# Kernel tuning notes

Hardware: AMD Instinct MI355X
Metric: run time of the kernel (lower is better)

Reference implementation:

```python
import jax, jax.numpy as jnp
import numpy as np
import math

EMBED = 512
KDIM = 512
VDIM = 512
H = 8
HD = EMBED // H
N = 2048
L = 2048
B = 4


def setup_inputs() -> dict:
    key = jax.random.key(0)
    ks = jax.random.split(key, 14)
    s = 1.0 / math.sqrt(EMBED)
    return {
        "q": jax.random.normal(ks[0], (N, B, EMBED), jnp.float32),
        "k": jax.random.normal(ks[1], (L, B, KDIM), jnp.float32),
        "v": jax.random.normal(ks[2], (L, B, VDIM), jnp.float32),
        "pe1": jax.random.normal(ks[3], (B, N, 3), jnp.float32),
        "pe2": jax.random.normal(ks[4], (L, 3), jnp.float32),
        "Wq": jax.random.normal(ks[5], (EMBED, EMBED), jnp.float32) * s,
        "bq": jnp.zeros((EMBED,), jnp.float32),
        "Wk": jax.random.normal(ks[6], (EMBED, KDIM), jnp.float32) * s,
        "bk": jnp.zeros((EMBED,), jnp.float32),
        "Wv": jax.random.normal(ks[7], (EMBED, VDIM), jnp.float32) * s,
        "bv": jnp.zeros((EMBED,), jnp.float32),
        "Wo": jax.random.normal(ks[8], (EMBED, EMBED), jnp.float32) * s,
        "bo": jnp.zeros((EMBED,), jnp.float32),
    }


def reference(q, k, v, pe1, pe2, Wq, bq, Wk, bk, Wv, bv, Wo, bo):
    n, b, _ = q.shape
    l = k.shape[0]
    # projections (nn.Linear: x @ W.T + b)
    qp = q @ Wq.T + bq  # (n, b, E)
    kp = k @ Wk.T + bk  # (l, b, E)
    vp = v @ Wv.T + bv  # (l, b, E)
    # split heads -> (b, H, n, hd)
    qh = qp.reshape(n, b, H, HD).transpose(1, 2, 0, 3)
    kh = kp.reshape(l, b, H, HD).transpose(1, 2, 0, 3)
    vh = vp.reshape(l, b, H, HD).transpose(1, 2, 0, 3)
    # relative PE bias: (b, n, l), broadcast over heads
    pe_scores = jnp.einsum('bnc,lc->bnl', pe1, pe2)[:, None, :, :]
    scores = (jnp.einsum('bhnd,bhld->bhnl', qh, kh) + pe_scores) / math.sqrt(HD)
    attn = jax.nn.softmax(scores, axis=-1)
    out = jnp.einsum('bhnl,bhld->bhnd', attn, vh)  # (b, H, n, hd)
    out = out.transpose(2, 0, 1, 3).reshape(n, b, EMBED)
    return out @ Wo.T + bo
```

## Files before the change

kernel.cpp:

```cpp
#include <hip/hip_runtime.h>
#include <math.h>

#define EMBED 512
#define HDIM 64
#define NHEADS 8
#define SEQ_N 2048
#define SEQ_L 2048
#define BATCH 4
#define MROWS (SEQ_N*BATCH)
#define BE (BATCH*EMBED)

#define QSCALE 0.18033688f

typedef _Float16 f16;
typedef _Float16 half8 __attribute__((ext_vector_type(8)));
typedef _Float16 half4 __attribute__((ext_vector_type(4)));
typedef _Float16 half2v __attribute__((ext_vector_type(2)));
typedef float floatx4 __attribute__((ext_vector_type(4)));
typedef float floatx16 __attribute__((ext_vector_type(16)));

static __device__ inline float fast_exp2(float x) {
#if __has_builtin(__builtin_amdgcn_exp2f)
  return __builtin_amdgcn_exp2f(x);
#else
  return __expf(x * 0.69314718056f);
#endif
}

static __device__ inline half2v pk2(float a, float b) {
#if __has_builtin(__builtin_amdgcn_cvt_pkrtz)
  return __builtin_bit_cast(half2v, __builtin_amdgcn_cvt_pkrtz(a, b));
#else
  half2v o; o[0] = (f16)a; o[1] = (f16)b; return o;
#endif
}

static __device__ inline void gload16(const void* g, void* l) {
  __builtin_amdgcn_global_load_lds(
      (__attribute__((address_space(1))) void*)(g),
      (__attribute__((address_space(3))) void*)(l), 16, 0, 0);
}

__global__ __launch_bounds__(256) void cvt_all(const float* __restrict__ q,
                                               const float* __restrict__ k,
                                               const float* __restrict__ v,
                                               const float* __restrict__ Wq,
                                               const float* __restrict__ Wk,
                                               const float* __restrict__ Wv,
                                               const float* __restrict__ Wo,
                                               f16* __restrict__ qb, f16* __restrict__ kb,
                                               f16* __restrict__ vb, f16* __restrict__ Wb) {
  const long TOK = (long)MROWS * EMBED;
  const long WSZ = (long)EMBED * EMBED;
  int y = blockIdx.y;
  long i = ((long)blockIdx.x * 256 + threadIdx.x) * 4;
  if (y < 3) {
    if (i < TOK) {
      const float* s = y == 0 ? q : y == 1 ? k : v;
      f16* d = y == 0 ? qb : y == 1 ? kb : vb;
      float4 f = *reinterpret_cast<const float4*>(s + i);
      half4 o; o[0] = (f16)f.x; o[1] = (f16)f.y; o[2] = (f16)f.z; o[3] = (f16)f.w;
      *reinterpret_cast<half4*>(d + i) = o;
    }
  } else {
    if (i < 4 * WSZ) {
      int sel = (int)(i >> 18);
      long off = i & (WSZ - 1);
      const float* s = sel == 0 ? Wq : sel == 1 ? Wk : sel == 2 ? Wv : Wo;
      float4 f = *reinterpret_cast<const float4*>(s + off);
      half4 o; o[0] = (f16)f.x; o[1] = (f16)f.y; o[2] = (f16)f.z; o[3] = (f16)f.w;
      *reinterpret_cast<half4*>(Wb + i) = o;
    }
  }
}

__global__ __launch_bounds__(256) void gemm_qkv(const f16* __restrict__ A0,
                                                const f16* __restrict__ A1,
                                                const f16* __restrict__ A2,
                                                const f16* __restrict__ W0,
                                                const f16* __restrict__ W1,
                                                const f16* __restrict__ W2,
                                                const float* __restrict__ b0,
                                                const float* __restrict__ b1,
                                                const float* __restrict__ b2,
                                                f16* __restrict__ C0, f16* __restrict__ C1,
                                                f16* __restrict__ C2t) {
  __shared__ alignas(16) unsigned char gsm[34816];
  f16* As = reinterpret_cast<f16*>(gsm);
  f16* Bs = reinterpret_cast<f16*>(gsm + 16384);
  f16* T  = reinterpret_cast<f16*>(gsm);
  const int sel = blockIdx.y >> 2;
  const f16* A = sel == 0 ? A0 : sel == 1 ? A1 : A2;
  const f16* Bt = sel == 0 ? W0 : sel == 1 ? W1 : W2;
  const float* bias = sel == 0 ? b0 : sel == 1 ? b1 : b2;
  const float scl = sel == 0 ? QSCALE : 1.0f;
  const int tid = threadIdx.x;
  const int wave = tid >> 6, lane = tid & 63, quad = lane >> 4, l16 = lane & 15;
  const int wm = wave & 1, wn = wave >> 1;
  const long m0 = (long)blockIdx.x * 128;
  const long n0 = (long)(blockIdx.y & 3) * 128;
  const int srow = lane >> 2;
  const int scol = (lane & 3) * 8;

  const f16* Ag0 = A + (m0 + wave * 32 + srow) * EMBED + scol;
  const f16* Ag1 = A + (m0 + wave * 32 + 16 + srow) * EMBED + scol;
  const f16* Bg0 = Bt + (n0 + wave * 32 + srow) * EMBED + scol;
  const f16* Bg1 = Bt + (n0 + wave * 32 + 16 + srow) * EMBED + scol;

  gload16(Ag0, &As[(wave * 32) * 32]);
  gload16(Ag1, &As[(wave * 32 + 16) * 32]);
  gload16(Bg0, &Bs[(wave * 32) * 32]);
  gload16(Bg1, &Bs[(wave * 32 + 16) * 32]);
  floatx4 acc[4][4] = {};
  asm volatile("s_waitcnt vmcnt(0)" ::: "memory");
  __builtin_amdgcn_s_barrier();

#pragma unroll
  for (int ks = 0; ks < 16; ++ks) {
    const int cur = ks & 1;
    if (ks + 1 < 16) {
      const int k1 = (ks + 1) * 32;
      gload16(Ag0 + k1, &As[(cur ^ 1) * 4096 + (wave * 32) * 32]);
      gload16(Ag1 + k1, &As[(cur ^ 1) * 4096 + (wave * 32 + 16) * 32]);
      gload16(Bg0 + k1, &Bs[(cur ^ 1) * 4096 + (wave * 32) * 32]);
      gload16(Bg1 + k1, &Bs[(cur ^ 1) * 4096 + (wave * 32 + 16) * 32]);
    }
    half8 af[4], bf[4];
#pragma unroll
    for (int i = 0; i < 4; ++i)
      af[i] = *reinterpret_cast<const half8*>(&As[cur * 4096 + (wm * 64 + i * 16 + l16) * 32 + quad * 8]);
#pragma unroll
    for (int j = 0; j < 4; ++j)
      bf[j] = *reinterpret_cast<const half8*>(&Bs[cur * 4096 + (wn * 64 + j * 16 + l16) * 32 + quad * 8]);
#pragma unroll
    for (int i = 0; i < 4; ++i)
#pragma unroll
      for (int j = 0; j < 4; ++j)
        acc[i][j] = __builtin_amdgcn_mfma_f32_16x16x32_f16(af[i], bf[j], acc[i][j], 0, 0, 0);
    if (ks + 1 < 16) {
      asm volatile("s_waitcnt vmcnt(0)" ::: "memory");
      __builtin_amdgcn_s_barrier();
    }
  }

  if (sel != 2) {
    f16* C = sel == 0 ? C0 : C1;
#pragma unroll
    for (int i = 0; i < 4; ++i)
#pragma unroll
      for (int r = 0; r < 4; ++r) {
        long row = m0 + wm * 64 + i * 16 + quad * 4 + r;
#pragma unroll
        for (int j = 0; j < 4; ++j) {
          long col = n0 + wn * 64 + j * 16 + l16;
          float val = (acc[i][j][r] + bias[col]) * scl;
          C[row * EMBED + col] = (f16)val;
        }
      }
  } else {
    __syncthreads();
#pragma unroll
    for (int i = 0; i < 4; ++i)
#pragma unroll
      for (int r = 0; r < 4; ++r) {
        int mrow = wm * 64 + i * 16 + quad * 4 + r;
        int bq = mrow & 3, lt = mrow >> 2;
#pragma unroll
        for (int j = 0; j < 4; ++j) {
          int col = wn * 64 + j * 16 + l16;
          float val = acc[i][j][r] + bias[n0 + col];
          T[col * 136 + bq * 32 + lt] = (f16)val;
        }
      }
    __syncthreads();
    const int h0 = (int)(n0 >> 6);
    const long lbase = m0 >> 2;
#pragma unroll
    for (int it = 0; it < 8; ++it) {
      int f = it * 256 + tid;
      int ls = f & 3, bq = (f >> 2) & 3, d6 = (f >> 4) & 63, hl = f >> 10;
      half8 o = *reinterpret_cast<const half8*>(&T[(hl * 64 + d6) * 136 + bq * 32 + ls * 8]);
      *reinterpret_cast<half8*>(C2t + (((long)bq * 8 + h0 + hl) * 64 + d6) * 2048 + lbase + ls * 8) = o;
    }
  }
}

__global__ __launch_bounds__(256) void gemm_out(const f16* __restrict__ A,
                                                const f16* __restrict__ Bt,
                                                const float* __restrict__ bias,
                                                float* __restrict__ C) {
  __shared__ alignas(16) f16 As[2][128 * 32];
  __shared__ alignas(16) f16 Bs[2][64 * 32];
  const int tid = threadIdx.x;
  const int wave = tid >> 6, lane = tid & 63, quad = lane >> 4, l16 = lane & 15;
  const long m0 = (long)blockIdx.x * 128;
  const long n0 = (long)blockIdx.y * 64;
  const int srow = lane >> 2;
  const int scol = (lane & 3) * 8;

  const f16* Ag0 = A + (m0 + wave * 32 + srow) * EMBED + scol;
  const f16* Ag1 = A + (m0 + wave * 32 + 16 + srow) * EMBED + scol;
  const f16* Bg0 = Bt + (n0 + wave * 16 + srow) * EMBED + scol;

  gload16(Ag0, &As[0][(wave * 32) * 32]);
  gload16(Ag1, &As[0][(wave * 32 + 16) * 32]);
  gload16(Bg0, &Bs[0][(wave * 16) * 32]);
  floatx4 acc[2][4] = {};
  asm volatile("s_waitcnt vmcnt(0)" ::: "memory");
  __builtin_amdgcn_s_barrier();

#pragma unroll
  for (int ks = 0; ks < 16; ++ks) {
    const int cur = ks & 1;
    if (ks + 1 < 16) {
      const int k1 = (ks + 1) * 32;
      gload16(Ag0 + k1, &As[cur ^ 1][(wave * 32) * 32]);
      gload16(Ag1 + k1, &As[cur ^ 1][(wave * 32 + 16) * 32]);
      gload16(Bg0 + k1, &Bs[cur ^ 1][(wave * 16) * 32]);
    }
    half8 af[2], bf[4];
#pragma unroll
    for (int i = 0; i < 2; ++i)
      af[i] = *reinterpret_cast<const half8*>(&As[cur][(wave * 32 + i * 16 + l16) * 32 + quad * 8]);
#pragma unroll
    for (int j = 0; j < 4; ++j)
      bf[j] = *reinterpret_cast<const half8*>(&Bs[cur][(j * 16 + l16) * 32 + quad * 8]);
#pragma unroll
    for (int i = 0; i < 2; ++i)
#pragma unroll
      for (int j = 0; j < 4; ++j)
        acc[i][j] = __builtin_amdgcn_mfma_f32_16x16x32_f16(af[i], bf[j], acc[i][j], 0, 0, 0);
    if (ks + 1 < 16) {
      asm volatile("s_waitcnt vmcnt(0)" ::: "memory");
      __builtin_amdgcn_s_barrier();
    }
  }
#pragma unroll
  for (int i = 0; i < 2; ++i)
#pragma unroll
    for (int r = 0; r < 4; ++r) {
      long row = m0 + wave * 32 + i * 16 + quad * 4 + r;
#pragma unroll
      for (int j = 0; j < 4; ++j) {
        long col = n0 + j * 16 + l16;
        C[row * EMBED + col] = acc[i][j][r] + bias[col];
      }
    }
}

#define KBUFB (128 * 64 * 2)
#define VBUFB (64 * 128 * 2)
#define PEBUFB (128 * 16 * 2)
#define LDSB (2 * KBUFB + 2 * VBUFB + 2 * PEBUFB)
#define NCHUNK (SEQ_L / 128)
__global__ __launch_bounds__(512, 4) void attn_flash(const f16* __restrict__ qp,
                                                     const f16* __restrict__ kp,
                                                     const f16* __restrict__ vt,
                                                     const float* __restrict__ pe1,
                                                     const float* __restrict__ pe2,
                                                     f16* __restrict__ ao) {
  __shared__ alignas(16) unsigned char smem[LDSB];
  f16* K0 = reinterpret_cast<f16*>(smem);
  f16* V0 = reinterpret_cast<f16*>(smem + 2 * KBUFB);
  f16* P0 = reinterpret_cast<f16*>(smem + 2 * KBUFB + 2 * VBUFB);
  float* comb = reinterpret_cast<float*>(smem);
  const int tid = threadIdx.x, wave = tid >> 6, lane = tid & 63;
  const int m = lane & 31, h = lane >> 5;
  const int strip = wave & 3, half = wave >> 2;
  const int W = blockIdx.y * 16 + blockIdx.x;
  const int bh = (W & 7) + ((W >> 7) << 3);
  const int n0 = ((W >> 3) & 15) * 128;
  const int b = bh >> 3, hd = bh & 7;
  const long headoff = (long)b * EMBED + hd * HDIM;
  const long vhead = (long)bh * 64 * 2048;

  const int krow0 = wave * 16 + (lane >> 3);
  const int kg = (lane & 7) ^ (lane >> 3);
  const f16* ksrc0 = kp + headoff + (long)krow0 * BE + kg * 8;
  const int vd0 = wave * 8 + (lane >> 4);
  const int vd1 = vd0 + 4;
  const int vg0 = (lane & 15) ^ (vd0 & 7);
  const int vg1 = (lane & 15) ^ (vd1 & 7);
  const f16* vsrc0 = vt + vhead + (long)vd0 * 2048 + vg0 * 8;
  const f16* vsrc1 = vt + vhead + (long)vd1 * 2048 + vg1 * 8;

  for (int c = tid; c < 1024; c += 512) {
    int r = c >> 3, col = (c & 7) * 8;
    *reinterpret_cast<uint4*>(&K0[r * 64 + col]) =
        *reinterpret_cast<const uint4*>(qp + (long)(n0 + r) * BE + headoff + col);
  }
  gload16(vsrc0, V0 + wave * 1024);
  gload16(vsrc1, V0 + wave * 1024 + 512);
  if (tid < 256) {
    const uint2 z2 = {0, 0};
    const uint4 z4 = {0, 0, 0, 0};
    *reinterpret_cast<uint2*>(reinterpret_cast<char*>(P0) + tid * 32 + 8) = z2;
    *reinterpret_cast<uint4*>(reinterpret_cast<char*>(P0) + tid * 32 + 16) = z4;
  }
  if (tid < 128) {
    long base = ((long)b * SEQ_N + n0 + tid) * 3;
    half4 v8;
    v8[0] = (f16)(pe1[base + 0] * QSCALE);
    v8[1] = (f16)(pe1[base + 1] * QSCALE);
    v8[2] = (f16)(pe1[base + 2] * QSCALE);
    v8[3] = (f16)0.f;
    *reinterpret_cast<half4*>(&P0[tid * 16]) = v8;
  }
  __syncthreads();

  half8 qf[5];
#pragma unroll
  for (int e = 0; e < 4; ++e)
    qf[e] = *reinterpret_cast<const half8*>(&K0[(strip * 32 + m) * 64 + e * 16 + h * 8]);
  qf[4] = *reinterpret_cast<const half8*>(&P0[(strip * 32 + m) * 16 + h * 8]);
  __syncthreads();

  gload16(ksrc0, K0 + wave * 1024);
  gload16(ksrc0 + 8 * BE, K0 + wave * 1024 + 512);
  {
    int pr = tid & 127;
    float a0 = pe2[(long)pr * 3 + 0];
    float a1 = pe2[(long)pr * 3 + 1];
    float a2 = pe2[(long)pr * 3 + 2];
    if (tid < 128) {
      half4 p2v; p2v[0] = (f16)a0; p2v[1] = (f16)a1; p2v[2] = (f16)a2; p2v[3] = (f16)0.f;
      *reinterpret_cast<half4*>(&P0[tid * 16]) = p2v;
    }
  }
  __syncthreads();

  floatx16 oacc[2] = {};
  float lpart = 0.f;

  auto compute_chunk = [&](int bsel) {
    const f16* Kb = K0 + bsel * 8192;
    const f16* Vb = V0 + bsel * 8192;
    const f16* Pb = P0 + bsel * 2048;
#pragma unroll
    for (int tt = 0; tt < 2; ++tt) {
      const int t = half * 2 + tt;
      const int row = t * 32 + m;
      const int r7 = m & 7;
      floatx16 st = {};
#pragma unroll
      for (int e = 0; e < 4; ++e) {
        half8 kf = *reinterpret_cast<const half8*>(&Kb[row * 64 + (((2 * e + h) ^ r7) * 8)]);
        st = __builtin_amdgcn_mfma_f32_32x32x16_f16(kf, qf[e], st, 0, 0, 0);
      }
      {
        half8 kf = *reinterpret_cast<const half8*>(&Pb[row * 16 + h * 8]);
        st = __builtin_amdgcn_mfma_f32_32x32x16_f16(kf, qf[4], st, 0, 0, 0);
      }
      float p[16];
#pragma unroll
      for (int r = 0; r < 16; ++r) {
        p[r] = fast_exp2(st[r]);
        lpart += p[r];
      }
#pragma unroll
      for (int s = 0; s < 4; ++s) {
        half2v u0 = pk2(p[4 * s + 0], p[4 * s + 1]);
        half2v u1 = pk2(p[4 * s + 2], p[4 * s + 3]);
        half4 bp;
        bp[0] = u0[0]; bp[1] = u0[1]; bp[2] = u1[0]; bp[3] = u1[1];
        const int sl = t * 4 + s;
#pragma unroll
        for (int dt = 0; dt < 2; ++dt) {
          const int d = dt * 32 + m;
          half4 vf = *reinterpret_cast<const half4*>(&Vb[d * 128 + ((sl ^ r7) * 8) + h * 4]);
          oacc[dt] = __builtin_amdgcn_mfma_f32_32x32x8f16(vf, bp, oacc[dt], 0, 0, 0);
        }
      }
    }
  };

  int buf = 0;
#pragma unroll 1
  for (int c = 0; c < NCHUNK - 1; ++c) {
    const int l0n = (c + 1) * 128;
    f16* Kn = K0 + (buf ^ 1) * 8192;
    f16* Vn = V0 + (buf ^ 1) * 8192;
    gload16(ksrc0 + (long)l0n * BE, Kn + wave * 1024);
    gload16(ksrc0 + (long)l0n * BE + 8 * BE, Kn + wave * 1024 + 512);
    gload16(vsrc0 + l0n, Vn + wave * 1024);
    gload16(vsrc1 + l0n, Vn + wave * 1024 + 512);
    int pr = tid & 127;
    float a0 = pe2[(long)(l0n + pr) * 3 + 0];
    float a1 = pe2[(long)(l0n + pr) * 3 + 1];
    float a2 = pe2[(long)(l0n + pr) * 3 + 2];

    __builtin_amdgcn_s_setprio(1);
    compute_chunk(buf);
    __builtin_amdgcn_s_setprio(0);

    if (tid < 128) {
      half4 p2v; p2v[0] = (f16)a0; p2v[1] = (f16)a1; p2v[2] = (f16)a2; p2v[3] = (f16)0.f;
      *reinterpret_cast<half4*>(&P0[(buf ^ 1) * 2048 + tid * 16]) = p2v;
    }
    __syncthreads();
    buf ^= 1;
  }
  __builtin_amdgcn_s_setprio(1);
  compute_chunk(buf);
  __builtin_amdgcn_s_setprio(0);
  __syncthreads();

  lpart += __shfl_xor(lpart, 32);

  if (half == 1) {
    float* dst = comb + (strip * 64 + lane) * 33;
#pragma unroll
    for (int dt = 0; dt < 2; ++dt)
#pragma unroll
      for (int x = 0; x < 16; ++x) dst[dt * 16 + x] = oacc[dt][x];
    dst[32] = lpart;
  }
  __syncthreads();
  if (half == 0) {
    const float* src = comb + (strip * 64 + lane) * 33;
#pragma unroll
    for (int dt = 0; dt < 2; ++dt)
#pragma unroll
      for (int x = 0; x < 16; ++x) oacc[dt][x] += src[dt * 16 + x];
    float inv = 1.f / (lpart + src[32]);
    long qrow = n0 + strip * 32 + m;
#pragma unroll
    for (int dt = 0; dt < 2; ++dt)
#pragma unroll
      for (int g = 0; g < 4; ++g) {
        half4 o4;
#pragma unroll
        for (int x = 0; x < 4; ++x) o4[x] = (f16)(oacc[dt][4 * g + x] * inv);
        int d = dt * 32 + 8 * g + 4 * h;
        *reinterpret_cast<half4*>(ao + qrow * BE + headoff + d) = o4;
      }
  }
}

extern "C" void kernel_launch(void* const* d_in, const int* in_sizes, int n_in,
                              void* d_out, int out_size, void* d_ws, size_t ws_size,
                              hipStream_t stream) {
  const float* q   = (const float*)d_in[0];
  const float* k   = (const float*)d_in[1];
  const float* v   = (const float*)d_in[2];
  const float* pe1 = (const float*)d_in[3];
  const float* pe2 = (const float*)d_in[4];
  const float* Wq  = (const float*)d_in[5];
  const float* bq  = (const float*)d_in[6];
  const float* Wk  = (const float*)d_in[7];
  const float* bk  = (const float*)d_in[8];
  const float* Wv  = (const float*)d_in[9];
  const float* bv  = (const float*)d_in[10];
  const float* Wo  = (const float*)d_in[11];
  const float* bo  = (const float*)d_in[12];
  float* out = (float*)d_out;

  f16* ws = (f16*)d_ws;
  const long TOK = (long)MROWS * EMBED;
  const long WSZ = (long)EMBED * EMBED;
  f16* qb  = ws;
  f16* kb  = qb + TOK;
  f16* vb  = kb + TOK;
  f16* Wqb = vb + TOK;
  f16* Wkb = Wqb + WSZ;
  f16* Wvb = Wkb + WSZ;
  f16* Wob = Wvb + WSZ;
  f16* qpb = Wob + WSZ;
  f16* kpb = qpb + TOK;
  f16* vtb = kpb + TOK;
  f16* aob = vtb + TOK;

  cvt_all<<<dim3(4096, 4), 256, 0, stream>>>(q, k, v, Wq, Wk, Wv, Wo, qb, kb, vb, Wqb);

  gemm_qkv<<<dim3(MROWS / 128, 12), 256, 0, stream>>>(qb, kb, vb, Wqb, Wkb, Wvb,
                                                      bq, bk, bv, qpb, kpb, vtb);

  attn_flash<<<dim3(SEQ_N / 128, BATCH * NHEADS), 512, 0, stream>>>(qpb, kpb, vtb, pe1, pe2, aob);

  gemm_out<<<dim3(MROWS / 128, EMBED / 64), 256, 0, stream>>>(aob, Wob, bo, out);
}
```

Baseline: 197.6 us.

## Fuse fp32-to-fp16 activation conversion into QKV GEMM loads

The QKV projection GEMM now reads the fp32 q/k/v activations directly into registers, converts them to fp16 and stores them into LDS. The separate conversion pass over the activations and its fp16 round trip through global memory are gone, leaving a small weight-only conversion kernel. Each GEMM block now re-reads fp32 A tiles, so with 4 column blocks per matrix that traffic repeats 4 times, and the A-tile pipeline moves from async global-to-LDS loads to register-staged stores. The s_setprio calls around the attention compute are also removed.

```diff
diff --git a/kernel.cpp b/kernel.cpp
--- a/kernel.cpp
+++ b/kernel.cpp
@@ -35,48 +35,39 @@
 #endif
 }
 
+static __device__ inline half8 cvt8(float4 u, float4 v) {
+  half2v p0 = pk2(u.x, u.y), p1 = pk2(u.z, u.w);
+  half2v p2 = pk2(v.x, v.y), p3 = pk2(v.z, v.w);
+  half8 o;
+  o[0] = p0[0]; o[1] = p0[1]; o[2] = p1[0]; o[3] = p1[1];
+  o[4] = p2[0]; o[5] = p2[1]; o[6] = p3[0]; o[7] = p3[1];
+  return o;
+}
+
 static __device__ inline void gload16(const void* g, void* l) {
   __builtin_amdgcn_global_load_lds(
       (__attribute__((address_space(1))) void*)(g),
       (__attribute__((address_space(3))) void*)(l), 16, 0, 0);
 }
 
-__global__ __launch_bounds__(256) void cvt_all(const float* __restrict__ q,
-                                               const float* __restrict__ k,
-                                               const float* __restrict__ v,
-                                               const float* __restrict__ Wq,
-                                               const float* __restrict__ Wk,
-                                               const float* __restrict__ Wv,
-                                               const float* __restrict__ Wo,
-                                               f16* __restrict__ qb, f16* __restrict__ kb,
-                                               f16* __restrict__ vb, f16* __restrict__ Wb) {
-  const long TOK = (long)MROWS * EMBED;
+__global__ __launch_bounds__(256) void cvt_w(const float* __restrict__ Wq,
+                                             const float* __restrict__ Wk,
+                                             const float* __restrict__ Wv,
+                                             const float* __restrict__ Wo,
+                                             f16* __restrict__ Wb) {
   const long WSZ = (long)EMBED * EMBED;
-  int y = blockIdx.y;
   long i = ((long)blockIdx.x * 256 + threadIdx.x) * 4;
-  if (y < 3) {
-    if (i < TOK) {
-      const float* s = y == 0 ? q : y == 1 ? k : v;
-      f16* d = y == 0 ? qb : y == 1 ? kb : vb;
-      float4 f = *reinterpret_cast<const float4*>(s + i);
-      half4 o; o[0] = (f16)f.x; o[1] = (f16)f.y; o[2] = (f16)f.z; o[3] = (f16)f.w;
-      *reinterpret_cast<half4*>(d + i) = o;
-    }
-  } else {
-    if (i < 4 * WSZ) {
-      int sel = (int)(i >> 18);
-      long off = i & (WSZ - 1);
-      const float* s = sel == 0 ? Wq : sel == 1 ? Wk : sel == 2 ? Wv : Wo;
-      float4 f = *reinterpret_cast<const float4*>(s + off);
-      half4 o; o[0] = (f16)f.x; o[1] = (f16)f.y; o[2] = (f16)f.z; o[3] = (f16)f.w;
-      *reinterpret_cast<half4*>(Wb + i) = o;
-    }
-  }
-}
-
-__global__ __launch_bounds__(256) void gemm_qkv(const f16* __restrict__ A0,
-                                                const f16* __restrict__ A1,
-                                                const f16* __restrict__ A2,
+  int sel = (int)(i >> 18);
+  long off = i & (WSZ - 1);
+  const float* s = sel == 0 ? Wq : sel == 1 ? Wk : sel == 2 ? Wv : Wo;
+  float4 f = *reinterpret_cast<const float4*>(s + off);
+  half4 o; o[0] = (f16)f.x; o[1] = (f16)f.y; o[2] = (f16)f.z; o[3] = (f16)f.w;
+  *reinterpret_cast<half4*>(Wb + i) = o;
+}
+
+__global__ __launch_bounds__(256) void gemm_qkv(const float* __restrict__ A0,
+                                                const float* __restrict__ A1,
+                                                const float* __restrict__ A2,
                                                 const f16* __restrict__ W0,
                                                 const f16* __restrict__ W1,
                                                 const f16* __restrict__ W2,
@@ -90,7 +81,7 @@
   f16* Bs = reinterpret_cast<f16*>(gsm + 16384);
   f16* T  = reinterpret_cast<f16*>(gsm);
   const int sel = blockIdx.y >> 2;
-  const f16* A = sel == 0 ? A0 : sel == 1 ? A1 : A2;
+  const float* A = sel == 0 ? A0 : sel == 1 ? A1 : A2;
   const f16* Bt = sel == 0 ? W0 : sel == 1 ? W1 : W2;
   const float* bias = sel == 0 ? b0 : sel == 1 ? b1 : b2;
   const float scl = sel == 0 ? QSCALE : 1.0f;
@@ -102,26 +93,34 @@
   const int srow = lane >> 2;
   const int scol = (lane & 3) * 8;
 
-  const f16* Ag0 = A + (m0 + wave * 32 + srow) * EMBED + scol;
-  const f16* Ag1 = A + (m0 + wave * 32 + 16 + srow) * EMBED + scol;
+  const int ar = tid >> 1;
+  const int ah = (tid & 1) * 16;
+  const float* Agp = A + (m0 + ar) * EMBED + ah;
   const f16* Bg0 = Bt + (n0 + wave * 32 + srow) * EMBED + scol;
   const f16* Bg1 = Bt + (n0 + wave * 32 + 16 + srow) * EMBED + scol;
 
-  gload16(Ag0, &As[(wave * 32) * 32]);
-  gload16(Ag1, &As[(wave * 32 + 16) * 32]);
-  gload16(Bg0, &Bs[(wave * 32) * 32]);
-  gload16(Bg1, &Bs[(wave * 32 + 16) * 32]);
+  {
+    float4 a4[4];
+#pragma unroll
+    for (int j = 0; j < 4; ++j)
+      a4[j] = *reinterpret_cast<const float4*>(Agp + j * 4);
+    gload16(Bg0, &Bs[(wave * 32) * 32]);
+    gload16(Bg1, &Bs[(wave * 32 + 16) * 32]);
+    *reinterpret_cast<half8*>(&As[ar * 32 + ah]) = cvt8(a4[0], a4[1]);
+    *reinterpret_cast<half8*>(&As[ar * 32 + ah + 8]) = cvt8(a4[2], a4[3]);
+  }
   floatx4 acc[4][4] = {};
-  asm volatile("s_waitcnt vmcnt(0)" ::: "memory");
-  __builtin_amdgcn_s_barrier();
+  __syncthreads();
 
 #pragma unroll
   for (int ks = 0; ks < 16; ++ks) {
     const int cur = ks & 1;
+    float4 a4[4];
     if (ks + 1 < 16) {
       const int k1 = (ks + 1) * 32;
-      gload16(Ag0 + k1, &As[(cur ^ 1) * 4096 + (wave * 32) * 32]);
-      gload16(Ag1 + k1, &As[(cur ^ 1) * 4096 + (wave * 32 + 16) * 32]);
+#pragma unroll
+      for (int j = 0; j < 4; ++j)
+        a4[j] = *reinterpret_cast<const float4*>(Agp + k1 + j * 4);
       gload16(Bg0 + k1, &Bs[(cur ^ 1) * 4096 + (wave * 32) * 32]);
       gload16(Bg1 + k1, &Bs[(cur ^ 1) * 4096 + (wave * 32 + 16) * 32]);
     }
@@ -138,8 +137,9 @@
       for (int j = 0; j < 4; ++j)
         acc[i][j] = __builtin_amdgcn_mfma_f32_16x16x32_f16(af[i], bf[j], acc[i][j], 0, 0, 0);
     if (ks + 1 < 16) {
-      asm volatile("s_waitcnt vmcnt(0)" ::: "memory");
-      __builtin_amdgcn_s_barrier();
+      *reinterpret_cast<half8*>(&As[(cur ^ 1) * 4096 + ar * 32 + ah]) = cvt8(a4[0], a4[1]);
+      *reinterpret_cast<half8*>(&As[(cur ^ 1) * 4096 + ar * 32 + ah + 8]) = cvt8(a4[2], a4[3]);
+      __syncthreads();
     }
   }
 
@@ -389,9 +389,7 @@
     float a1 = pe2[(long)(l0n + pr) * 3 + 1];
     float a2 = pe2[(long)(l0n + pr) * 3 + 2];
 
-    __builtin_amdgcn_s_setprio(1);
     compute_chunk(buf);
-    __builtin_amdgcn_s_setprio(0);
 
     if (tid < 128) {
       half4 p2v; p2v[0] = (f16)a0; p2v[1] = (f16)a1; p2v[2] = (f16)a2; p2v[3] = (f16)0.f;
@@ -400,9 +398,7 @@
     __syncthreads();
     buf ^= 1;
   }
-  __builtin_amdgcn_s_setprio(1);
   compute_chunk(buf);
-  __builtin_amdgcn_s_setprio(0);
   __syncthreads();
 
   lpart += __shfl_xor(lpart, 32);
@@ -458,10 +454,7 @@
   f16* ws = (f16*)d_ws;
   const long TOK = (long)MROWS * EMBED;
   const long WSZ = (long)EMBED * EMBED;
-  f16* qb  = ws;
-  f16* kb  = qb + TOK;
-  f16* vb  = kb + TOK;
-  f16* Wqb = vb + TOK;
+  f16* Wqb = ws;
   f16* Wkb = Wqb + WSZ;
   f16* Wvb = Wkb + WSZ;
   f16* Wob = Wvb + WSZ;
@@ -470,9 +463,9 @@
   f16* vtb = kpb + TOK;
   f16* aob = vtb + TOK;
 
-  cvt_all<<<dim3(4096, 4), 256, 0, stream>>>(q, k, v, Wq, Wk, Wv, Wo, qb, kb, vb, Wqb);
-
-  gemm_qkv<<<dim3(MROWS / 128, 12), 256, 0, stream>>>(qb, kb, vb, Wqb, Wkb, Wvb,
+  cvt_w<<<dim3(1024), 256, 0, stream>>>(Wq, Wk, Wv, Wo, Wqb);
+
+  gemm_qkv<<<dim3(MROWS / 128, 12), 256, 0, stream>>>(q, k, v, Wqb, Wkb, Wvb,
                                                       bq, bk, bv, qpb, kpb, vtb);
 
   attn_flash<<<dim3(SEQ_N / 128, BATCH * NHEADS), 512, 0, stream>>>(qpb, kpb, vtb, pe1, pe2, aob);
```

New measurement: 208.7 us. +5.6%, slower.
